# Kernel tuning notes

Measured on AMD Instinct MI355X. Metric: run time of the kernel, lower is better.

Reference implementation:

```python
import jax, jax.numpy as jnp
import numpy as np

B, S, W = 64, 128, 16
VOCAB, CVOCAB = 50000, 100
WDIM, CDIM, NF = 300, 50, 50
KS = [3, 4, 5]
HID, NLAYERS, NLAB = 256, 2, 5
COMB = WDIM + NF * len(KS)  # 450


def glorot(key, shape):
    fan_in, fan_out = shape[-2], shape[-1]
    lim = jnp.sqrt(6.0 / (fan_in + fan_out))
    return jax.random.uniform(key, shape, minval=-lim, maxval=lim, dtype=jnp.float32)


def setup_inputs() -> dict:
    key = jax.random.key(0)
    ks = jax.random.split(key, 32)
    word_ids = jax.random.randint(ks[0], (B, S), 1, VOCAB)
    char_ids = jax.random.randint(ks[1], (B, S, W), 1, CVOCAB)
    labels = jax.random.randint(ks[2], (B, S), 0, NLAB)
    lengths = jax.random.randint(ks[3], (B,), S // 2, S + 1)
    # embeddings
    word_emb = jax.random.normal(ks[4], (VOCAB, WDIM), jnp.float32) * 0.1
    word_emb = word_emb.at[0].set(0.0)
    char_emb = jax.random.normal(ks[5], (CVOCAB, CDIM), jnp.float32) * 0.1
    char_emb = char_emb.at[0].set(0.0)
    # char conv kernels: [ks, CDIM, NF] each, plus bias
    conv_w = [glorot(ks[6 + i], (k, CDIM, NF)) for i, k in enumerate(KS)]
    conv_b = [jnp.zeros((NF,), jnp.float32) for _ in KS]
    # LSTM params per layer per direction: W_ih [in,4H], W_hh [H,4H], b [4H]
    lstm = []
    kidx = 10
    in_dim = COMB
    for layer in range(NLAYERS):
        for d in range(2):
            Wih = glorot(ks[kidx], (in_dim, 4 * HID)); kidx += 1
            Whh = glorot(ks[kidx], (HID, 4 * HID)); kidx += 1
            b = jnp.zeros((4 * HID,), jnp.float32)
            lstm.extend([Wih, Whh, b])
        in_dim = 2 * HID
    out_w = glorot(ks[kidx], (2 * HID, NLAB)); kidx += 1
    out_b = jnp.zeros((NLAB,), jnp.float32)
    crf_start = jax.random.normal(ks[kidx], (NLAB,), jnp.float32) * 0.1; kidx += 1
    crf_end = jax.random.normal(ks[kidx], (NLAB,), jnp.float32) * 0.1; kidx += 1
    crf_trans = jax.random.normal(ks[kidx], (NLAB, NLAB), jnp.float32) * 0.1
    d = {
        'word_ids': word_ids, 'char_ids': char_ids, 'labels': labels, 'lengths': lengths,
        'word_emb': word_emb, 'char_emb': char_emb,
        'conv_w3': conv_w[0], 'conv_b3': conv_b[0],
        'conv_w4': conv_w[1], 'conv_b4': conv_b[1],
        'conv_w5': conv_w[2], 'conv_b5': conv_b[2],
        'out_w': out_w, 'out_b': out_b,
        'crf_start': crf_start, 'crf_end': crf_end, 'crf_trans': crf_trans,
    }
    names = ['Wih', 'Whh', 'b']
    i = 0
    for layer in range(NLAYERS):
        for dname in ['f', 'r']:
            for n in names:
                d[f'lstm_{n}_l{layer}{dname}'] = lstm[i]; i += 1
    return d


def _conv1d_same(x, w, b, pad):
    # x: [N, L, Cin], w: [k, Cin, Cout] -> [N, L_out, Cout]
    out = jax.lax.conv_general_dilated(x, w, window_strides=(1,), padding=[(pad, pad)],
                                       dimension_numbers=('NWC', 'WIO', 'NWC'))
    return out + b


def _lstm_dir(x, Wih, Whh, b, reverse):
    # x: [B, S, in] -> [B, S, H]; gate order i,f,g,o (torch convention)
    xg = jnp.einsum('bsi,ij->bsj', x, Wih) + b  # [B,S,4H]
    if reverse:
        xg = xg[:, ::-1]
    def step(carry, g):
        h, c = carry
        g = g + h @ Whh
        i, f, gg, o = jnp.split(g, 4, axis=-1)
        i, f, o = jax.nn.sigmoid(i), jax.nn.sigmoid(f), jax.nn.sigmoid(o)
        c = f * c + i * jnp.tanh(gg)
        h = o * jnp.tanh(c)
        return (h, c), h
    h0 = jnp.zeros((x.shape[0], HID), x.dtype)
    _, hs = jax.lax.scan(step, (h0, h0), jnp.swapaxes(xg, 0, 1))
    hs = jnp.swapaxes(hs, 0, 1)
    if reverse:
        hs = hs[:, ::-1]
    return hs


def reference(word_ids, char_ids, labels, lengths, word_emb, char_emb,
              conv_w3, conv_b3, conv_w4, conv_b4, conv_w5, conv_b5,
              out_w, out_b, crf_start, crf_end, crf_trans,
              lstm_Wih_l0f, lstm_Whh_l0f, lstm_b_l0f,
              lstm_Wih_l0r, lstm_Whh_l0r, lstm_b_l0r,
              lstm_Wih_l1f, lstm_Whh_l1f, lstm_b_l1f,
              lstm_Wih_l1r, lstm_Whh_l1r, lstm_b_l1r):
    # char CNN
    ce = char_emb[char_ids.reshape(-1, W)]  # [B*S, W, CDIM]
    pooled = []
    for w, b, k in [(conv_w3, conv_b3, 3), (conv_w4, conv_b4, 4), (conv_w5, conv_b5, 5)]:
        o = jax.nn.relu(_conv1d_same(ce, w, b, k // 2))
        pooled.append(jnp.max(o, axis=1))  # [B*S, NF]
    char_repr = jnp.concatenate(pooled, axis=-1).reshape(B, S, NF * len(KS))
    we = word_emb[word_ids]
    x = jnp.concatenate([we, char_repr], axis=-1)  # [B,S,COMB]
    # BiLSTM 2 layers (dropout disabled / eval mode)
    h_f = _lstm_dir(x, lstm_Wih_l0f, lstm_Whh_l0f, lstm_b_l0f, False)
    h_r = _lstm_dir(x, lstm_Wih_l0r, lstm_Whh_l0r, lstm_b_l0r, True)
    x = jnp.concatenate([h_f, h_r], axis=-1)
    h_f = _lstm_dir(x, lstm_Wih_l1f, lstm_Whh_l1f, lstm_b_l1f, False)
    h_r = _lstm_dir(x, lstm_Wih_l1r, lstm_Whh_l1r, lstm_b_l1r, True)
    x = jnp.concatenate([h_f, h_r], axis=-1)
    emissions = jnp.einsum('bsh,hl->bsl', x, out_w) + out_b  # [B,S,NLAB]
    # CRF NLL (pytorch-crf, batch_first, reduction='mean')
    mask = (jnp.arange(S)[None, :] < lengths[:, None])  # [B,S] bool
    maskf = mask.astype(emissions.dtype)
    tags = labels  # already in [0,NLAB)
    # numerator: score of gold path
    em_score = jnp.take_along_axis(emissions, tags[..., None], axis=-1)[..., 0]  # [B,S]
    num = crf_start[tags[:, 0]] + em_score[:, 0]
    trans_score = crf_trans[tags[:, :-1], tags[:, 1:]]  # [B,S-1]
    num = num + jnp.sum((trans_score + em_score[:, 1:]) * maskf[:, 1:], axis=1)
    last_idx = lengths - 1
    last_tag = jnp.take_along_axis(tags, last_idx[:, None], axis=1)[:, 0]
    num = num + crf_end[last_tag]
    # denominator: forward algorithm via scan
    alpha0 = crf_start + emissions[:, 0]  # [B,NLAB]
    def step(alpha, inp):
        em_t, m_t = inp  # [B,NLAB], [B]
        nxt = jax.nn.logsumexp(alpha[:, :, None] + crf_trans[None], axis=1) + em_t
        alpha = jnp.where(m_t[:, None], nxt, alpha)
        return alpha, None
    alpha, _ = jax.lax.scan(step, alpha0,
                            (jnp.swapaxes(emissions[:, 1:], 0, 1), jnp.swapaxes(mask[:, 1:], 0, 1)))
    denom = jax.nn.logsumexp(alpha + crf_end[None], axis=1)  # [B]
    llh = num - denom
    return -jnp.mean(llh)
```

## Files before the change

### kernel.cpp

```cpp
#include <hip/hip_runtime.h>
#include <hip/hip_fp16.h>
#include <math.h>
#include <stdint.h>

#define NB   64
#define NS   128
#define NW   16
#define CD   50
#define NF_  50
#define WD   300
#define COMB 450
#define K2P0 240
#define K2P1 256
#define HID  256
#define G4   1024
#define NLAB 5

#define WHH_SW4  (7.0f / 0.06846532f)
#define WHH_INV4 (1.0f / (WHH_SW4 * 7.0f))

#define CW_S   (7.0f / 0.24494897f)
#define EMB_S  14.0f
#define CONV_INV (1.0f / (CW_S * EMB_S))

typedef _Float16 h2_t __attribute__((ext_vector_type(2)));
typedef _Float16 v8h  __attribute__((ext_vector_type(8)));
typedef float    v16f __attribute__((ext_vector_type(16)));

__device__ __forceinline__ float sigf(float x)   { return 1.0f / (1.0f + __expf(-x)); }
__device__ __forceinline__ float tanhf_(float x) { return 1.0f - 2.0f / (__expf(2.0f * x) + 1.0f); }

__device__ __forceinline__ int sdot8f(uint32_t a, int b, int acc) {
#if __has_builtin(__builtin_amdgcn_sdot8)
    return __builtin_amdgcn_sdot8((int)a, b, acc, false);
#else
#pragma unroll
    for (int i = 0; i < 8; ++i) {
        int av = ((int)(a << (28 - 4 * i))) >> 28;
        int bv = ((int)(((uint32_t)b) << (28 - 4 * i))) >> 28;
        acc += av * bv;
    }
    return acc;
#endif
}

__device__ __forceinline__ uint32_t packh2(float lo, float hi) {
    __half l = __float2half(lo), h = __float2half(hi);
    return ((uint32_t)__half_as_ushort(h) << 16) | (uint32_t)__half_as_ushort(l);
}

__device__ __forceinline__ int q4clamp(float v, float s) {
    int q = (int)rintf(v * s);
    return q < -7 ? -7 : (q > 7 ? 7 : q);
}

#define PK_CONV_END 17
#define PK_WIH0_END (17 + 1920)
#define PK_WIH1_END (PK_WIH0_END + 2048)
#define PK_END      (PK_WIH1_END + 512)

__global__ __launch_bounds__(256) void pack_all(
    const float* __restrict__ w3, const float* __restrict__ w4,
    const float* __restrict__ w5, uint32_t* __restrict__ cwq,
    const float* __restrict__ Wih0f, const float* __restrict__ Wih0r,
    const float* __restrict__ Wih1f, const float* __restrict__ Wih1r,
    uint32_t* __restrict__ P0f, uint32_t* __restrict__ P0r,
    uint32_t* __restrict__ P1f, uint32_t* __restrict__ P1r,
    const float* __restrict__ Whh0f, const float* __restrict__ Whh0r,
    const float* __restrict__ Whh1f, const float* __restrict__ Whh1r,
    uint32_t* __restrict__ Q0f, uint32_t* __restrict__ Q0r,
    uint32_t* __restrict__ Q1f, uint32_t* __restrict__ Q1r)
{
    int blk = blockIdx.x;
    int tid = threadIdx.x;

    if (blk < PK_CONV_END) {
        int idx = blk * 256 + tid;
        if (idx >= 4200) return;
        const float* W; int rel;
        if (idx < 1050)       { W = w3; rel = idx; }
        else if (idx < 2450)  { W = w4; rel = idx - 1050; }
        else                  { W = w5; rel = idx - 2450; }
        int t = rel / 350, r2 = rel - t * 350;
        int wi = r2 / 50, f = r2 - wi * 50;
        uint32_t out = 0;
#pragma unroll
        for (int j = 0; j < 8; ++j) {
            int c = wi * 8 + j;
            if (c < CD) {
                int q = q4clamp(W[(size_t)(t * CD + c) * NF_ + f], CW_S);
                out |= ((uint32_t)(q & 0xF)) << (4 * j);
            }
        }
        cwq[idx] = out;
    } else if (blk < PK_WIH1_END) {
        int layer, dir, rel;
        if (blk < PK_WIH0_END) { layer = 0; rel = blk - PK_CONV_END; dir = rel / 960;  rel %= 960; }
        else                   { layer = 1; rel = blk - PK_WIH0_END; dir = rel / 1024; rel %= 1024; }
        int K   = layer ? 512 : COMB;
        int K2P = layer ? K2P1 : K2P0;
        const float* W = layer ? (dir ? Wih1r : Wih1f) : (dir ? Wih0r : Wih0f);
        uint32_t* P    = layer ? (dir ? P1r : P1f) : (dir ? P0r : P0f);
        int idx = rel * 256 + tid;
        if (idx >= K2P * 1024) return;
        int n = idx & 1023, kp = idx >> 10;
        uint32_t v = 0;
        if (2 * kp + 1 < K) {
            __half l = __float2half(W[(size_t)(2 * kp) * 1024 + n]);
            __half h = __float2half(W[(size_t)(2 * kp + 1) * 1024 + n]);
            v = ((uint32_t)__half_as_ushort(h) << 16) | (uint32_t)__half_as_ushort(l);
        }
        P[((size_t)(kp >> 2) * 1024 + n) * 4 + (kp & 3)] = v;
    } else {
        int rel = blk - PK_WIH1_END;
        int which = rel >> 7;
        const float* W; uint32_t* Q;
        switch (which) {
            case 0:  W = Whh0f; Q = Q0f; break;
            case 1:  W = Whh0r; Q = Q0r; break;
            case 2:  W = Whh1f; Q = Q1f; break;
            default: W = Whh1r; Q = Q1r; break;
        }
        int idx = (rel & 127) * 256 + tid;
        int m = idx & 3, col = (idx >> 2) & 1023, iq = idx >> 12;
        int kbase = (iq * 4 + m) * 8;
        uint32_t out = 0;
#pragma unroll
        for (int j = 0; j < 8; ++j) {
            int q = q4clamp(W[(size_t)(kbase + j) * G4 + col], WHH_SW4);
            out |= ((uint32_t)(q & 0xF)) << (4 * j);
        }
        Q[idx] = out;
    }
}

__global__ __launch_bounds__(512) void cnn_embed4(
    const int* __restrict__ word_ids, const int* __restrict__ char_ids,
    const float* __restrict__ word_emb, const float* __restrict__ char_emb,
    const uint32_t* __restrict__ cwq,
    const float* __restrict__ b3, const float* __restrict__ b4,
    const float* __restrict__ b5, uint32_t* __restrict__ x0p)
{
    __shared__ uint32_t cws[4200];
    __shared__ uint32_t cepq[8][NW][7];
    int tid  = threadIdx.x;
    int g    = tid >> 6;
    int lane = tid & 63;
    int pos  = blockIdx.x * 8 + g;

    for (int i = tid; i < 4200; i += 512) cws[i] = cwq[i];

    const int* cid = char_ids + (size_t)pos * NW;
    for (int idx = lane; idx < NW * 7; idx += 64) {
        int w  = idx / 7;
        int wi = idx - w * 7;
        const float* e = char_emb + (size_t)cid[w] * CD + 8 * wi;
        int nc = CD - 8 * wi; if (nc > 8) nc = 8;
        uint32_t pk = 0;
        for (int j = 0; j < nc; ++j) {
            float v = e[j];
            v = v > 0.5f ? 0.5f : (v < -0.5f ? -0.5f : v);
            int q = q4clamp(v, EMB_S);
            pk |= ((uint32_t)(q & 0xF)) << (4 * j);
        }
        cepq[g][w][wi] = pk;
    }
    {
        int wid = word_ids[pos];
        const float* src = word_emb + (size_t)wid * WD;
        uint32_t* dst = x0p + (size_t)pos * K2P0;
        for (int idx = lane; idx < 150; idx += 64) {
            float2 v = *(const float2*)(src + 2 * idx);
            dst[idx] = packh2(v.x, v.y);
        }
        for (int idx = lane; idx < 15; idx += 64) dst[225 + idx] = 0;
    }
    __syncthreads();

    int f = lane;
    float m3 = 0.f, m4 = 0.f, m5 = 0.f;
    if (f < NF_) {
        int a3[16] = {}, a4[17] = {}, a5[16] = {};
        for (int wi = 0; wi < 7; ++wi) {
            uint32_t w3q[3], w4q[4], w5q[5];
#pragma unroll
            for (int t = 0; t < 3; ++t) w3q[t] = cws[(t * 7 + wi) * NF_ + f];
#pragma unroll
            for (int t = 0; t < 4; ++t) w4q[t] = cws[1050 + (t * 7 + wi) * NF_ + f];
#pragma unroll
            for (int t = 0; t < 5; ++t) w5q[t] = cws[2450 + (t * 7 + wi) * NF_ + f];
#pragma unroll
            for (int ip = 0; ip < 16; ++ip) {
                uint32_t e = cepq[g][ip][wi];
#pragma unroll
                for (int t = 0; t < 3; ++t) { int p = ip + 1 - t; if (p >= 0 && p < 16) a3[p] = sdot8f(e, (int)w3q[t], a3[p]); }
#pragma unroll
                for (int t = 0; t < 4; ++t) { int p = ip + 2 - t; if (p >= 0 && p < 17) a4[p] = sdot8f(e, (int)w4q[t], a4[p]); }
#pragma unroll
                for (int t = 0; t < 5; ++t) { int p = ip + 2 - t; if (p >= 0 && p < 16) a5[p] = sdot8f(e, (int)w5q[t], a5[p]); }
            }
        }
        int i3 = a3[0], i4 = a4[0], i5 = a5[0];
#pragma unroll
        for (int p = 1; p < 16; ++p) { i3 = max(i3, a3[p]); i5 = max(i5, a5[p]); }
#pragma unroll
        for (int p = 1; p < 17; ++p) i4 = max(i4, a4[p]);
        m3 = fmaxf(0.f, (float)i3 * CONV_INV + b3[f]);
        m4 = fmaxf(0.f, (float)i4 * CONV_INV + b4[f]);
        m5 = fmaxf(0.f, (float)i5 * CONV_INV + b5[f]);
    }
    float m3x = __shfl_xor(m3, 1);
    float m4x = __shfl_xor(m4, 1);
    float m5x = __shfl_xor(m5, 1);
    if (f < NF_ && !(f & 1)) {
        int i = f >> 1;
        uint32_t* dst = x0p + (size_t)pos * K2P0 + 150;
        dst[i]      = packh2(m3, m3x);
        dst[25 + i] = packh2(m4, m4x);
        dst[50 + i] = packh2(m5, m5x);
    }
}

__global__ __launch_bounds__(256) void gemm_mfma(
    const uint32_t* __restrict__ Ap, int K2,
    const uint32_t* __restrict__ Wpf, const uint32_t* __restrict__ Wpr,
    const float* __restrict__ bf, const float* __restrict__ br,
    float* __restrict__ Cf, float* __restrict__ Cr)
{
    int by  = blockIdx.y;
    int dir = by >> 4;
    int n0  = (by & 15) * 64;
    int m0  = blockIdx.x * 128;
    const uint32_t* Wp = dir ? Wpr : Wpf;
    const float* bias  = dir ? br : bf;
    float* C           = dir ? Cr : Cf;

    int tid = threadIdx.x;
    int w = tid >> 6, l = tid & 63;
    int l31 = l & 31, lk = l >> 5;

    const uint32_t* arow = Ap + (size_t)(m0 + w * 32 + l31) * K2 + lk * 4;
    const uint4*    bq0  = (const uint4*)(Wp) + (size_t)lk * 1024 + n0 + l31;

    v16f acc0 = {}, acc1 = {};

    for (int kp0 = 0; kp0 < K2; kp0 += 8) {
        uint4 av = *(const uint4*)(arow + kp0);
        const uint4* bq = bq0 + (size_t)(kp0 >> 2) * 1024;
        uint4 b0v = bq[0];
        uint4 b1v = bq[32];
        v8h af = __builtin_bit_cast(v8h, av);
        acc0 = __builtin_amdgcn_mfma_f32_32x32x16_f16(af, __builtin_bit_cast(v8h, b0v), acc0, 0, 0, 0);
        acc1 = __builtin_amdgcn_mfma_f32_32x32x16_f16(af, __builtin_bit_cast(v8h, b1v), acc1, 0, 0, 0);
    }

#pragma unroll
    for (int r = 0; r < 16; ++r) {
        int row = m0 + w * 32 + (r & 3) + 8 * (r >> 2) + 4 * lk;
        int c0 = n0 + l31, c1 = n0 + 32 + l31;
        C[(size_t)row * G4 + c0] = acc0[r] + bias[c0];
        C[(size_t)row * G4 + c1] = acc1[r] + bias[c1];
    }
}

__global__ __launch_bounds__(512, 1) void lstm_rec17(
    const float* __restrict__ xg_f, const float* __restrict__ xg_r,
    const uint32_t* __restrict__ Qf, const uint32_t* __restrict__ Qr,
    uint32_t* __restrict__ outp)
{
    int bid = blockIdx.x;
    int b = bid >> 1, d = bid & 1;
    const float* xg = d ? xg_r : xg_f;
    const uint4* Q4 = (const uint4*)(d ? Qr : Qf);

    __shared__ uint32_t hp8[32];
    __shared__ float gates[G4];

    int t = threadIdx.x;
    int lane = t & 63;

    uint4 rA[8], rB[8];
#pragma unroll
    for (int iq = 0; iq < 8; ++iq) {
        rA[iq] = Q4[(size_t)iq * 1024 + t];
        rB[iq] = Q4[(size_t)iq * 1024 + t + 512];
    }
    if (t < 32) hp8[t] = 0;
    float cst = 0.f;

    int te0 = d ? (NS - 1) : 0;
    size_t prow = ((size_t)b * NS + te0) * G4;
    float xA = xg[prow + t];
    float xB = xg[prow + 512 + t];
    __syncthreads();

    for (int s = 0; s < NS; ++s) {
        int te = d ? (NS - 1 - s) : s;
        int row = b * NS + te;

        float nxA = 0.f, nxB = 0.f;
        if (s + 1 < NS) {
            int te1 = d ? (NS - 2 - s) : (s + 1);
            size_t r1 = ((size_t)b * NS + te1) * G4;
            nxA = xg[r1 + t];
            nxB = xg[r1 + 512 + t];
        }

        int hreg = (int)hp8[lane & 31];
        int a0 = 0, a0b = 0, a1 = 0, a1b = 0;

#pragma unroll
        for (int iq = 0; iq < 8; ++iq) {
            int h0 = __builtin_amdgcn_readlane(hreg, 4 * iq);
            int h1 = __builtin_amdgcn_readlane(hreg, 4 * iq + 1);
            int h2 = __builtin_amdgcn_readlane(hreg, 4 * iq + 2);
            int h3 = __builtin_amdgcn_readlane(hreg, 4 * iq + 3);
            a0  = sdot8f(rA[iq].x, h0, a0);  a0b = sdot8f(rA[iq].y, h1, a0b);
            a0  = sdot8f(rA[iq].z, h2, a0);  a0b = sdot8f(rA[iq].w, h3, a0b);
            a1  = sdot8f(rB[iq].x, h0, a1);  a1b = sdot8f(rB[iq].y, h1, a1b);
            a1  = sdot8f(rB[iq].z, h2, a1);  a1b = sdot8f(rB[iq].w, h3, a1b);
        }

        gates[t]       = (float)(a0 + a0b) * WHH_INV4 + xA;
        gates[t + 512] = (float)(a1 + a1b) * WHH_INV4 + xB;
        __syncthreads();
        if (t < 256) {
            int j = t;
            float gi = gates[j];
            float gf = gates[256 + j];
            float gg = gates[512 + j];
            float go = gates[768 + j];
            float ii = sigf(gi), ff = sigf(gf), g2 = tanhf_(gg), oo = sigf(go);
            cst = ff * cst + ii * g2;
            float h = oo * tanhf_(cst);
            int q = (int)rintf(h * 7.0f);
            q = q < -7 ? -7 : (q > 7 ? 7 : q);
            int qx = __shfl_xor(q, 1);
            float hx = __shfl_xor(h, 1);
            if (!(t & 1)) {
                ((unsigned char*)hp8)[j >> 1] =
                    (unsigned char)((q & 0xF) | ((qx & 0xF) << 4));
                outp[(size_t)row * 256 + d * 128 + (j >> 1)] = packh2(h, hx);
            }
        }
        xA = nxA; xB = nxB;
        __syncthreads();
    }
}

__global__ __launch_bounds__(256) void emis_kernel2(
    const uint32_t* __restrict__ x2p, const float* __restrict__ ow,
    const float* __restrict__ ob, float* __restrict__ em)
{
    __shared__ float ows[2560];
    __shared__ float obs[NLAB];
    int tid = threadIdx.x;
    for (int i = tid; i < 2560; i += 256) ows[i] = ow[i];
    if (tid < NLAB) obs[tid] = ob[tid];
    __syncthreads();

    int wv = tid >> 6, lane = tid & 63;
    int row = blockIdx.x * 4 + wv;
    const uint32_t* xr = x2p + (size_t)row * 256;

    float acc[NLAB] = {};
#pragma unroll
    for (int m = 0; m < 4; ++m) {
        int p = lane + 64 * m;
        h2_t hv = __builtin_bit_cast(h2_t, xr[p]);
        float lo = (float)hv[0], hi = (float)hv[1];
        int k = 2 * p;
#pragma unroll
        for (int l = 0; l < NLAB; ++l)
            acc[l] += lo * ows[k * NLAB + l] + hi * ows[(k + 1) * NLAB + l];
    }
#pragma unroll
    for (int off = 32; off > 0; off >>= 1)
#pragma unroll
        for (int l = 0; l < NLAB; ++l) acc[l] += __shfl_down(acc[l], off);
    if (lane < NLAB) {  }
    if (lane == 0) {
#pragma unroll
        for (int l = 0; l < NLAB; ++l)
            em[(size_t)row * NLAB + l] = acc[l] + obs[l];
    }
}

__device__ __forceinline__ float lse5(const float* v) {
    float m = fmaxf(fmaxf(fmaxf(v[0], v[1]), fmaxf(v[2], v[3])), v[4]);
    float s = __expf(v[0] - m) + __expf(v[1] - m) + __expf(v[2] - m) +
              __expf(v[3] - m) + __expf(v[4] - m);
    return m + __logf(s);
}

__global__ __launch_bounds__(64) void crf_kernel(
    const float* __restrict__ em, const int* __restrict__ labels,
    const int* __restrict__ lengths, const float* __restrict__ cstart,
    const float* __restrict__ cend, const float* __restrict__ ctrans,
    float* __restrict__ outp)
{
    __shared__ float tr_s[25], st_s[5], en_s[5];
    int tid = threadIdx.x;
    if (tid < 25) tr_s[tid] = ctrans[tid];
    if (tid < 5)  { st_s[tid] = cstart[tid]; en_s[tid] = cend[tid]; }
    __syncthreads();

    int b = tid;
    int len = lengths[b];
    const int* tg = labels + (size_t)b * NS;
    const float* eb = em + (size_t)b * NS * NLAB;

    int prev = tg[0];
    float num = st_s[prev] + eb[prev];
    for (int t = 1; t < NS; ++t) {
        if (t < len) {
            int cur = tg[t];
            num += tr_s[prev * NLAB + cur] + eb[t * NLAB + cur];
            prev = cur;
        }
    }
    num += en_s[tg[len - 1]];

    float a[NLAB];
#pragma unroll
    for (int y = 0; y < NLAB; ++y) a[y] = st_s[y] + eb[y];
    for (int t = 1; t < NS; ++t) {
        if (t < len) {
            float na[NLAB];
#pragma unroll
            for (int y = 0; y < NLAB; ++y) {
                float v[NLAB];
#pragma unroll
                for (int x = 0; x < NLAB; ++x) v[x] = a[x] + tr_s[x * NLAB + y];
                na[y] = lse5(v) + eb[t * NLAB + y];
            }
#pragma unroll
            for (int y = 0; y < NLAB; ++y) a[y] = na[y];
        }
    }
    float v[NLAB];
#pragma unroll
    for (int y = 0; y < NLAB; ++y) v[y] = a[y] + en_s[y];
    float denom = lse5(v);

    float llh = num - denom;
#pragma unroll
    for (int off = 32; off > 0; off >>= 1) llh += __shfl_down(llh, off);
    if (tid == 0) outp[0] = -llh * (1.0f / 64.0f);
}

extern "C" void kernel_launch(void* const* d_in, const int* in_sizes, int n_in,
                              void* d_out, int out_size, void* d_ws, size_t ws_size,
                              hipStream_t stream)
{
    const int*   word_ids = (const int*)d_in[0];
    const int*   char_ids = (const int*)d_in[1];
    const int*   labels   = (const int*)d_in[2];
    const int*   lengths  = (const int*)d_in[3];
    const float* word_emb = (const float*)d_in[4];
    const float* char_emb = (const float*)d_in[5];
    const float* cw3 = (const float*)d_in[6];
    const float* cb3 = (const float*)d_in[7];
    const float* cw4 = (const float*)d_in[8];
    const float* cb4 = (const float*)d_in[9];
    const float* cw5 = (const float*)d_in[10];
    const float* cb5 = (const float*)d_in[11];
    const float* out_w = (const float*)d_in[12];
    const float* out_b = (const float*)d_in[13];
    const float* crf_start = (const float*)d_in[14];
    const float* crf_end   = (const float*)d_in[15];
    const float* crf_trans = (const float*)d_in[16];
    const float* Wih_l0f = (const float*)d_in[17];
    const float* Whh_l0f = (const float*)d_in[18];
    const float* b_l0f   = (const float*)d_in[19];
    const float* Wih_l0r = (const float*)d_in[20];
    const float* Whh_l0r = (const float*)d_in[21];
    const float* b_l0r   = (const float*)d_in[22];
    const float* Wih_l1f = (const float*)d_in[23];
    const float* Whh_l1f = (const float*)d_in[24];
    const float* b_l1f   = (const float*)d_in[25];
    const float* Wih_l1r = (const float*)d_in[26];
    const float* Whh_l1r = (const float*)d_in[27];
    const float* b_l1r   = (const float*)d_in[28];

    uint32_t* wsu = (uint32_t*)d_ws;
    uint32_t* x0p  = wsu;
    float*    xg_f = (float*)(wsu + 1966080);
    float*    xg_r = xg_f + 8388608;
    uint32_t* x1p  = (uint32_t*)(xg_r + 8388608);
    uint32_t* x2p  = x1p + 2097152;
    float*    em   = (float*)(x2p + 2097152);
    uint32_t* wp0f = (uint32_t*)(em + 40960);
    uint32_t* wp0r = wp0f + 245760;
    uint32_t* wp1f = wp0r + 245760;
    uint32_t* wp1r = wp1f + 262144;
    uint32_t* cwq  = wp1r + 262144;
    uint32_t* wh0f = cwq  + 4200;
    uint32_t* wh0r = wh0f + 32768;
    uint32_t* wh1f = wh0r + 32768;
    uint32_t* wh1r = wh1f + 32768;

    pack_all<<<PK_END, 256, 0, stream>>>(
        cw3, cw4, cw5, cwq,
        Wih_l0f, Wih_l0r, Wih_l1f, Wih_l1r, wp0f, wp0r, wp1f, wp1r,
        Whh_l0f, Whh_l0r, Whh_l1f, Whh_l1r, wh0f, wh0r, wh1f, wh1r);

    cnn_embed4<<<1024, 512, 0, stream>>>(word_ids, char_ids, word_emb, char_emb,
                                         cwq, cb3, cb4, cb5, x0p);

    dim3 gGemm(64, 32);
    gemm_mfma<<<gGemm, 256, 0, stream>>>(x0p, K2P0, wp0f, wp0r, b_l0f, b_l0r, xg_f, xg_r);

    lstm_rec17<<<128, 512, 0, stream>>>(xg_f, xg_r, wh0f, wh0r, x1p);

    gemm_mfma<<<gGemm, 256, 0, stream>>>(x1p, K2P1, wp1f, wp1r, b_l1f, b_l1r, xg_f, xg_r);

    lstm_rec17<<<128, 512, 0, stream>>>(xg_f, xg_r, wh1f, wh1r, x2p);

    emis_kernel2<<<2048, 256, 0, stream>>>(x2p, out_w, out_b, em);
    crf_kernel<<<1, 64, 0, stream>>>(em, labels, lengths, crf_start, crf_end, crf_trans,
                                     (float*)d_out);
}
```

Measured before the change: 454.5 us.

## Fuse weight packing into CNN embed kernel and widen GEMM N-tile

Merges the separate weight-packing kernel and the char-CNN embedding kernel into one launch. Each CNN block now quantizes the conv weights straight into shared memory, so the global cwq buffer and one launch go away, while the remaining blocks pack the LSTM weights. Separately, the input-projection GEMM now covers 128 output columns per block with four MFMA accumulators instead of two, which reuses each A load across more columns and halves the grid. The cost is redundant conv-weight quantization in every CNN block, plus higher register pressure in the GEMM.

```diff
diff --git a/kernel.cpp b/kernel.cpp
--- a/kernel.cpp
+++ b/kernel.cpp
@@ -54,14 +54,18 @@
     return q < -7 ? -7 : (q > 7 ? 7 : q);
 }
 
-#define PK_CONV_END 17
-#define PK_WIH0_END (17 + 1920)
-#define PK_WIH1_END (PK_WIH0_END + 2048)
-#define PK_END      (PK_WIH1_END + 512)
-
-__global__ __launch_bounds__(256) void pack_all(
+#define PREP_CNN_END  1024
+#define PREP_WIH0_END (PREP_CNN_END + 960)
+#define PREP_WIH1_END (PREP_WIH0_END + 1024)
+#define PREP_END      (PREP_WIH1_END + 256)
+
+__global__ __launch_bounds__(512) void prep_kernel(
+    const int* __restrict__ word_ids, const int* __restrict__ char_ids,
+    const float* __restrict__ word_emb, const float* __restrict__ char_emb,
     const float* __restrict__ w3, const float* __restrict__ w4,
-    const float* __restrict__ w5, uint32_t* __restrict__ cwq,
+    const float* __restrict__ w5,
+    const float* __restrict__ b3, const float* __restrict__ b4,
+    const float* __restrict__ b5, uint32_t* __restrict__ x0p,
     const float* __restrict__ Wih0f, const float* __restrict__ Wih0r,
     const float* __restrict__ Wih1f, const float* __restrict__ Wih1r,
     uint32_t* __restrict__ P0f, uint32_t* __restrict__ P0r,
@@ -74,13 +78,61 @@
     int blk = blockIdx.x;
     int tid = threadIdx.x;
 
-    if (blk < PK_CONV_END) {
-        int idx = blk * 256 + tid;
-        if (idx >= 4200) return;
+    if (blk >= PREP_CNN_END) {
+        if (blk < PREP_WIH1_END) {
+            int layer = (blk >= PREP_WIH0_END);
+            int base  = layer ? PREP_WIH0_END : PREP_CNN_END;
+            int K     = layer ? 512 : COMB;
+            int K2P   = layer ? K2P1 : K2P0;
+            int span  = K2P * 1024;
+            int idx = (blk - base) * 512 + tid;
+            int dir = idx >= span;
+            int sub = idx - dir * span;
+            const float* W = layer ? (dir ? Wih1r : Wih1f) : (dir ? Wih0r : Wih0f);
+            uint32_t* P    = layer ? (dir ? P1r : P1f) : (dir ? P0r : P0f);
+            int n = sub & 1023, kp = sub >> 10;
+            uint32_t v = 0;
+            if (2 * kp + 1 < K) {
+                __half l = __float2half(W[(size_t)(2 * kp) * 1024 + n]);
+                __half h = __float2half(W[(size_t)(2 * kp + 1) * 1024 + n]);
+                v = ((uint32_t)__half_as_ushort(h) << 16) | (uint32_t)__half_as_ushort(l);
+            }
+            P[((size_t)(kp >> 2) * 1024 + n) * 4 + (kp & 3)] = v;
+        } else {
+            int idx = (blk - PREP_WIH1_END) * 512 + tid;
+            int which = idx >> 15;
+            int sub = idx & 32767;
+            const float* W; uint32_t* Q;
+            switch (which) {
+                case 0:  W = Whh0f; Q = Q0f; break;
+                case 1:  W = Whh0r; Q = Q0r; break;
+                case 2:  W = Whh1f; Q = Q1f; break;
+                default: W = Whh1r; Q = Q1r; break;
+            }
+            int m = sub & 3, col = (sub >> 2) & 1023, iq = sub >> 12;
+            int kbase = (iq * 4 + m) * 8;
+            uint32_t out = 0;
+#pragma unroll
+            for (int j = 0; j < 8; ++j) {
+                int q = q4clamp(W[(size_t)(kbase + j) * G4 + col], WHH_SW4);
+                out |= ((uint32_t)(q & 0xF)) << (4 * j);
+            }
+            Q[sub] = out;
+        }
+        return;
+    }
+
+    __shared__ uint32_t cws[4200];
+    __shared__ uint32_t cepq[8][NW][7];
+    int g    = tid >> 6;
+    int lane = tid & 63;
+    int pos  = blk * 8 + g;
+
+    for (int i = tid; i < 4200; i += 512) {
         const float* W; int rel;
-        if (idx < 1050)       { W = w3; rel = idx; }
-        else if (idx < 2450)  { W = w4; rel = idx - 1050; }
-        else                  { W = w5; rel = idx - 2450; }
+        if (i < 1050)       { W = w3; rel = i; }
+        else if (i < 2450)  { W = w4; rel = i - 1050; }
+        else                { W = w5; rel = i - 2450; }
         int t = rel / 350, r2 = rel - t * 350;
         int wi = r2 / 50, f = r2 - wi * 50;
         uint32_t out = 0;
@@ -92,63 +144,8 @@
                 out |= ((uint32_t)(q & 0xF)) << (4 * j);
             }
         }
-        cwq[idx] = out;
-    } else if (blk < PK_WIH1_END) {
-        int layer, dir, rel;
-        if (blk < PK_WIH0_END) { layer = 0; rel = blk - PK_CONV_END; dir = rel / 960;  rel %= 960; }
-        else                   { layer = 1; rel = blk - PK_WIH0_END; dir = rel / 1024; rel %= 1024; }
-        int K   = layer ? 512 : COMB;
-        int K2P = layer ? K2P1 : K2P0;
-        const float* W = layer ? (dir ? Wih1r : Wih1f) : (dir ? Wih0r : Wih0f);
-        uint32_t* P    = layer ? (dir ? P1r : P1f) : (dir ? P0r : P0f);
-        int idx = rel * 256 + tid;
-        if (idx >= K2P * 1024) return;
-        int n = idx & 1023, kp = idx >> 10;
-        uint32_t v = 0;
-        if (2 * kp + 1 < K) {
-            __half l = __float2half(W[(size_t)(2 * kp) * 1024 + n]);
-            __half h = __float2half(W[(size_t)(2 * kp + 1) * 1024 + n]);
-            v = ((uint32_t)__half_as_ushort(h) << 16) | (uint32_t)__half_as_ushort(l);
-        }
-        P[((size_t)(kp >> 2) * 1024 + n) * 4 + (kp & 3)] = v;
-    } else {
-        int rel = blk - PK_WIH1_END;
-        int which = rel >> 7;
-        const float* W; uint32_t* Q;
-        switch (which) {
-            case 0:  W = Whh0f; Q = Q0f; break;
-            case 1:  W = Whh0r; Q = Q0r; break;
-            case 2:  W = Whh1f; Q = Q1f; break;
-            default: W = Whh1r; Q = Q1r; break;
-        }
-        int idx = (rel & 127) * 256 + tid;
-        int m = idx & 3, col = (idx >> 2) & 1023, iq = idx >> 12;
-        int kbase = (iq * 4 + m) * 8;
-        uint32_t out = 0;
-#pragma unroll
-        for (int j = 0; j < 8; ++j) {
-            int q = q4clamp(W[(size_t)(kbase + j) * G4 + col], WHH_SW4);
-            out |= ((uint32_t)(q & 0xF)) << (4 * j);
-        }
-        Q[idx] = out;
-    }
-}
-
-__global__ __launch_bounds__(512) void cnn_embed4(
-    const int* __restrict__ word_ids, const int* __restrict__ char_ids,
-    const float* __restrict__ word_emb, const float* __restrict__ char_emb,
-    const uint32_t* __restrict__ cwq,
-    const float* __restrict__ b3, const float* __restrict__ b4,
-    const float* __restrict__ b5, uint32_t* __restrict__ x0p)
-{
-    __shared__ uint32_t cws[4200];
-    __shared__ uint32_t cepq[8][NW][7];
-    int tid  = threadIdx.x;
-    int g    = tid >> 6;
-    int lane = tid & 63;
-    int pos  = blockIdx.x * 8 + g;
-
-    for (int i = tid; i < 4200; i += 512) cws[i] = cwq[i];
+        cws[i] = out;
+    }
 
     const int* cid = char_ids + (size_t)pos * NW;
     for (int idx = lane; idx < NW * 7; idx += 64) {
@@ -221,15 +218,15 @@
     }
 }
 
-__global__ __launch_bounds__(256) void gemm_mfma(
+__global__ __launch_bounds__(256) void gemm_mfma2(
     const uint32_t* __restrict__ Ap, int K2,
     const uint32_t* __restrict__ Wpf, const uint32_t* __restrict__ Wpr,
     const float* __restrict__ bf, const float* __restrict__ br,
     float* __restrict__ Cf, float* __restrict__ Cr)
 {
     int by  = blockIdx.y;
-    int dir = by >> 4;
-    int n0  = (by & 15) * 64;
+    int dir = by >> 3;
+    int n0  = (by & 7) * 128;
     int m0  = blockIdx.x * 128;
     const uint32_t* Wp = dir ? Wpr : Wpf;
     const float* bias  = dir ? br : bf;
@@ -242,24 +239,32 @@
     const uint32_t* arow = Ap + (size_t)(m0 + w * 32 + l31) * K2 + lk * 4;
     const uint4*    bq0  = (const uint4*)(Wp) + (size_t)lk * 1024 + n0 + l31;
 
-    v16f acc0 = {}, acc1 = {};
+    v16f acc0 = {}, acc1 = {}, acc2 = {}, acc3 = {};
 
     for (int kp0 = 0; kp0 < K2; kp0 += 8) {
         uint4 av = *(const uint4*)(arow + kp0);
         const uint4* bq = bq0 + (size_t)(kp0 >> 2) * 1024;
         uint4 b0v = bq[0];
         uint4 b1v = bq[32];
+        uint4 b2v = bq[64];
+        uint4 b3v = bq[96];
         v8h af = __builtin_bit_cast(v8h, av);
         acc0 = __builtin_amdgcn_mfma_f32_32x32x16_f16(af, __builtin_bit_cast(v8h, b0v), acc0, 0, 0, 0);
         acc1 = __builtin_amdgcn_mfma_f32_32x32x16_f16(af, __builtin_bit_cast(v8h, b1v), acc1, 0, 0, 0);
-    }
-
+        acc2 = __builtin_amdgcn_mfma_f32_32x32x16_f16(af, __builtin_bit_cast(v8h, b2v), acc2, 0, 0, 0);
+        acc3 = __builtin_amdgcn_mfma_f32_32x32x16_f16(af, __builtin_bit_cast(v8h, b3v), acc3, 0, 0, 0);
+    }
+
+    int c0 = n0 + l31, c1 = n0 + 32 + l31, c2 = n0 + 64 + l31, c3 = n0 + 96 + l31;
+    float bb0 = bias[c0], bb1 = bias[c1], bb2 = bias[c2], bb3 = bias[c3];
 #pragma unroll
     for (int r = 0; r < 16; ++r) {
         int row = m0 + w * 32 + (r & 3) + 8 * (r >> 2) + 4 * lk;
-        int c0 = n0 + l31, c1 = n0 + 32 + l31;
-        C[(size_t)row * G4 + c0] = acc0[r] + bias[c0];
-        C[(size_t)row * G4 + c1] = acc1[r] + bias[c1];
+        float* crow = C + (size_t)row * G4;
+        crow[c0] = acc0[r] + bb0;
+        crow[c1] = acc1[r] + bb1;
+        crow[c2] = acc2[r] + bb2;
+        crow[c3] = acc3[r] + bb3;
     }
 }
 
@@ -378,7 +383,6 @@
     for (int off = 32; off > 0; off >>= 1)
 #pragma unroll
         for (int l = 0; l < NLAB; ++l) acc[l] += __shfl_down(acc[l], off);
-    if (lane < NLAB) {  }
     if (lane == 0) {
 #pragma unroll
         for (int l = 0; l < NLAB; ++l)
@@ -494,26 +498,23 @@
     uint32_t* wp0r = wp0f + 245760;
     uint32_t* wp1f = wp0r + 245760;
     uint32_t* wp1r = wp1f + 262144;
-    uint32_t* cwq  = wp1r + 262144;
-    uint32_t* wh0f = cwq  + 4200;
+    uint32_t* wh0f = wp1r + 262144;
     uint32_t* wh0r = wh0f + 32768;
     uint32_t* wh1f = wh0r + 32768;
     uint32_t* wh1r = wh1f + 32768;
 
-    pack_all<<<PK_END, 256, 0, stream>>>(
-        cw3, cw4, cw5, cwq,
+    prep_kernel<<<PREP_END, 512, 0, stream>>>(
+        word_ids, char_ids, word_emb, char_emb,
+        cw3, cw4, cw5, cb3, cb4, cb5, x0p,
         Wih_l0f, Wih_l0r, Wih_l1f, Wih_l1r, wp0f, wp0r, wp1f, wp1r,
         Whh_l0f, Whh_l0r, Whh_l1f, Whh_l1r, wh0f, wh0r, wh1f, wh1r);
 
-    cnn_embed4<<<1024, 512, 0, stream>>>(word_ids, char_ids, word_emb, char_emb,
-                                         cwq, cb3, cb4, cb5, x0p);
-
-    dim3 gGemm(64, 32);
-    gemm_mfma<<<gGemm, 256, 0, stream>>>(x0p, K2P0, wp0f, wp0r, b_l0f, b_l0r, xg_f, xg_r);
+    dim3 gGemm(64, 16);
+    gemm_mfma2<<<gGemm, 256, 0, stream>>>(x0p, K2P0, wp0f, wp0r, b_l0f, b_l0r, xg_f, xg_r);
 
     lstm_rec17<<<128, 512, 0, stream>>>(xg_f, xg_r, wh0f, wh0r, x1p);
 
-    gemm_mfma<<<gGemm, 256, 0, stream>>>(x1p, K2P1, wp1f, wp1r, b_l1f, b_l1r, xg_f, xg_r);
+    gemm_mfma2<<<gGemm, 256, 0, stream>>>(x1p, K2P1, wp1f, wp1r, b_l1f, b_l1r, xg_f, xg_r);
 
     lstm_rec17<<<128, 512, 0, stream>>>(xg_f, xg_r, wh1f, wh1r, x2p);
 
```

After: 466.4 us. 2.6% more time.
